# Optimization experiments

Hardware: AMD Instinct MI355X
Metric: run time of the kernel (lower is better)

The kernel has to match this reference:

```python
import jax, jax.numpy as jnp
import numpy as np

NUM_HEADS = 8
SIZES = [(80, 80), (40, 40), (20, 20), (10, 10), (5, 5)]


def _ln(x, g, b):
    m = x.mean(-1, keepdims=True)
    var = ((x - m) ** 2).mean(-1, keepdims=True)
    return (x - m) / jnp.sqrt(var + 1e-5) * g + b


def setup_inputs() -> dict:
    key = jax.random.key(0)
    ks = jax.random.split(key, 24)
    bs, c, S = 2, 256, 1024  # v_dim = embed_dim = c
    d = {}
    for i, (h, w) in enumerate(SIZES):
        d[f"q{i}"] = jax.random.normal(ks[i], (bs, c, h, w), jnp.float32)
    d["cache"] = jax.random.normal(ks[5], (bs, S, c), jnp.float32)
    d["mask"] = jax.random.randint(ks[6], (bs, S), 0, 2).astype(jnp.int32)
    d["ln_v_g"] = jnp.ones((c,), jnp.float32)
    d["ln_v_b"] = jnp.zeros((c,), jnp.float32)
    d["ln_c_g"] = jnp.ones((c,), jnp.float32)
    d["ln_c_b"] = jnp.zeros((c,), jnp.float32)
    sd = c ** -0.5
    d["Wv"] = jax.random.normal(ks[7], (c, c), jnp.float32) * sd
    d["bv"] = jnp.zeros((c,), jnp.float32)
    d["Wc"] = jax.random.normal(ks[8], (c, c), jnp.float32) * sd
    d["bc"] = jnp.zeros((c,), jnp.float32)
    d["Wvc"] = jax.random.normal(ks[9], (c, c), jnp.float32) * sd
    d["bvc"] = jnp.zeros((c,), jnp.float32)
    d["Wo"] = jax.random.normal(ks[10], (c, c), jnp.float32) * sd
    d["bo"] = jnp.zeros((c,), jnp.float32)
    d["Wg1"] = jax.random.normal(ks[11], (c, c // 2), jnp.float32) * sd
    d["bg1"] = jnp.zeros((c // 2,), jnp.float32)
    d["Wg2"] = jax.random.normal(ks[12], (c // 2, c), jnp.float32) * 0.01
    d["bg2"] = jnp.zeros((c,), jnp.float32)
    return d


def _forward(q0, q1, q2, q3, q4, cache, mask, ln_v_g, ln_v_b, ln_c_g, ln_c_b,
             Wv, bv, Wc, bc, Wvc, bvc, Wo, bo, Wg1, bg1, Wg2, bg2):
    feats = [q0, q1, q2, q3, q4]
    bs = q0.shape[0]
    sizes = [(f.shape[2], f.shape[3]) for f in feats]
    # permute_and_flatten: (bs, c, h, w) -> (bs, h*w, c), concat over levels
    v = jnp.concatenate(
        [f.reshape(bs, f.shape[1], -1).transpose(0, 2, 1) for f in feats], axis=1)
    T = v.shape[1]
    E = Wv.shape[1]
    hd = E // NUM_HEADS
    scale = hd ** -0.5

    vn = _ln(v, ln_v_g, ln_v_b)
    cn = _ln(cache, ln_c_g, ln_c_b)

    q = ((vn @ Wv + bv) * scale).reshape(bs, T, NUM_HEADS, hd).transpose(0, 2, 1, 3)
    k = (cn @ Wc + bc).reshape(bs, -1, NUM_HEADS, hd).transpose(0, 2, 1, 3)
    val = (cn @ Wvc + bvc).reshape(bs, -1, NUM_HEADS, hd).transpose(0, 2, 1, 3)

    attn = jnp.einsum('bhtd,bhsd->bhts', q, k)
    attn = jnp.clip(attn, -50000.0, 50000.0)
    mf = mask.astype(attn.dtype)  # (bs, S); zeros -> -9e15, ones kept as +1.0 (faithful)
    attn = attn + jnp.where(mf == 0, jnp.asarray(-9e15, attn.dtype), mf)[:, None, None, :]
    p = jax.nn.softmax(attn, axis=-1)  # dropout inactive in eval mode

    o = jnp.einsum('bhts,bhsd->bhtd', p, val).transpose(0, 2, 1, 3).reshape(bs, T, E)
    delta = o @ Wo + bo

    gate = jnp.tanh(jax.nn.relu(v @ Wg1 + bg1) @ Wg2 + bg2)
    new_v = (v + gate * delta).transpose(0, 2, 1)  # (bs, c, T)

    outs = []
    start = 0
    for h, w in sizes:
        outs.append(new_v[:, :, start:start + h * w].reshape(bs, -1, h, w))
        start += h * w
    return tuple(outs)


def reference(q0, q1, q2, q3, q4, cache, mask, ln_v_g, ln_v_b, ln_c_g, ln_c_b,
              Wv, bv, Wc, bc, Wvc, bvc, Wo, bo, Wg1, bg1, Wg2, bg2):
    return _forward(q0, q1, q2, q3, q4, cache, mask, ln_v_g, ln_v_b, ln_c_g, ln_c_b,
                    Wv, bv, Wc, bc, Wvc, bvc, Wo, bo, Wg1, bg1, Wg2, bg2)
```

## Files before the change

### kernel.cpp

```cpp
#include <hip/hip_runtime.h>
#include <hip/hip_bf16.h>
#include <math.h>


typedef __attribute__((ext_vector_type(8))) short short8;
typedef __attribute__((ext_vector_type(4))) float f32x4;
typedef __hip_bfloat16 bf16;

#define T_TOK 8525
#define S_TOK 1024
#define CDIM  256
#define NHEAD 8
#define BSZ   2

static __device__ __forceinline__ f32x4 mfma16(short8 a, short8 b, f32x4 c) {
  return __builtin_amdgcn_mfma_f32_16x16x32_bf16(a, b, c, 0, 0, 0);
}

static __device__ __forceinline__ float fexp2(float x) {
#if __has_builtin(__builtin_amdgcn_exp2f)
  return __builtin_amdgcn_exp2f(x);
#else
  return exp2f(x);
#endif
}

static __device__ __forceinline__ unsigned int pack_bf16(float a, float b) {
#if __has_builtin(__builtin_amdgcn_perm)
  return __builtin_amdgcn_perm(__float_as_uint(b), __float_as_uint(a), 0x07060302u);
#else
  return (__float_as_uint(a) >> 16) | (__float_as_uint(b) & 0xFFFF0000u);
#endif
}

__global__ __launch_bounds__(256) void prep_misc(
    const float* __restrict__ Wv, const float* __restrict__ Wc,
    const float* __restrict__ Wvc, const float* __restrict__ Wo,
    const float* __restrict__ Wg1, const float* __restrict__ Wg2,
    const float* __restrict__ bc, const float* __restrict__ bvc,
    const float* __restrict__ cache, const float* __restrict__ ln_c_g,
    const float* __restrict__ ln_c_b,
    bf16* __restrict__ WvT, bf16* __restrict__ WcvcT, bf16* __restrict__ WoT,
    bf16* __restrict__ Wg1T, bf16* __restrict__ Wg2T, float* __restrict__ biasCV,
    bf16* __restrict__ cnb) {
  const int bid = blockIdx.x, tid = threadIdx.x;
  if (bid == 80) {
    biasCV[tid] = bc[tid];
    biasCV[tid + 256] = bvc[tid];
    return;
  }
  if (bid > 80) {
    int lane = tid & 63;
    int row = (bid - 81) * 4 + (tid >> 6);
    const float* x = cache + (size_t)row * CDIM;
    float v0 = x[lane], v1 = x[lane + 64], v2 = x[lane + 128], v3 = x[lane + 192];
    float s = v0 + v1 + v2 + v3;
    float s2 = v0 * v0 + v1 * v1 + v2 * v2 + v3 * v3;
#pragma unroll
    for (int off = 1; off < 64; off <<= 1) {
      s += __shfl_xor(s, off);
      s2 += __shfl_xor(s2, off);
    }
    float mean = s * (1.f / 256.f);
    float var = s2 * (1.f / 256.f) - mean * mean;
    float rstd = rsqrtf(var + 1e-5f);
    bf16* y = cnb + (size_t)row * CDIM;
    y[lane] = __float2bfloat16((v0 - mean) * rstd * ln_c_g[lane] + ln_c_b[lane]);
    y[lane + 64] = __float2bfloat16((v1 - mean) * rstd * ln_c_g[lane + 64] + ln_c_b[lane + 64]);
    y[lane + 128] = __float2bfloat16((v2 - mean) * rstd * ln_c_g[lane + 128] + ln_c_b[lane + 128]);
    y[lane + 192] = __float2bfloat16((v3 - mean) * rstd * ln_c_g[lane + 192] + ln_c_b[lane + 192]);
    return;
  }
  const float* W; bf16* WT; int K, N, local;
  if (bid < 16)      { W = Wv;  WT = WvT;           K = 256; N = 256; local = bid; }
  else if (bid < 32) { W = Wc;  WT = WcvcT;         K = 256; N = 256; local = bid - 16; }
  else if (bid < 48) { W = Wvc; WT = WcvcT + 65536; K = 256; N = 256; local = bid - 32; }
  else if (bid < 64) { W = Wo;  WT = WoT;           K = 256; N = 256; local = bid - 48; }
  else if (bid < 72) { W = Wg1; WT = Wg1T;          K = 256; N = 128; local = bid - 64; }
  else               { W = Wg2; WT = Wg2T;          K = 128; N = 256; local = bid - 72; }
  const int ktiles = K >> 6;
  const int K0 = (local % ktiles) * 64, N0 = (local / ktiles) * 64;
  __shared__ float tl[64][65];
  const int kk = tid >> 4, n4 = (tid & 15) * 4;
#pragma unroll
  for (int i = 0; i < 4; ++i) {
    int k = kk + 16 * i;
    float4 w4 = *(const float4*)&W[(size_t)(K0 + k) * N + N0 + n4];
    tl[n4 + 0][k] = w4.x; tl[n4 + 1][k] = w4.y;
    tl[n4 + 2][k] = w4.z; tl[n4 + 3][k] = w4.w;
  }
  __syncthreads();
  const int nn = tid >> 4, k4 = (tid & 15) * 4;
#pragma unroll
  for (int i = 0; i < 4; ++i) {
    int n = nn + 16 * i;
    bf16 o[4] __attribute__((aligned(8)));
#pragma unroll
    for (int j = 0; j < 4; ++j) o[j] = __float2bfloat16(tl[n][k4 + j]);
    *(uint2*)&WT[(size_t)(N0 + n) * K + K0 + k4] = *(uint2*)o;
  }
}

__global__ __launch_bounds__(256) void build_v_ln(
    const float* __restrict__ q0, const float* __restrict__ q1,
    const float* __restrict__ q2, const float* __restrict__ q3,
    const float* __restrict__ q4, const float* __restrict__ g,
    const float* __restrict__ beta, float* __restrict__ vT,
    bf16* __restrict__ vb, bf16* __restrict__ vnb) {
  constexpr int HW[5] = {6400, 1600, 400, 100, 25};
  constexpr int TST[5] = {0, 6400, 8000, 8400, 8500};
  constexpr int T16[5] = {0, 400, 500, 525, 532};
  __shared__ float tile[16][260];
  const int tid = threadIdx.x;
  const int tileid = blockIdx.x, b = blockIdx.y;
  int lvl = 0;
#pragma unroll
  for (int i = 1; i < 5; ++i) if (tileid >= T16[i]) lvl = i;
  const int p0 = (tileid - T16[lvl]) * 16;
  const int hw = HW[lvl];
  const float* src = ((lvl == 0) ? q0 : (lvl == 1) ? q1 : (lvl == 2) ? q2
                      : (lvl == 3) ? q3 : q4) + (size_t)b * CDIM * hw;
  const int pl = tid & 15, cb = tid >> 4;
  const int pg = p0 + pl;
#pragma unroll
  for (int i = 0; i < 16; ++i) {
    int c = cb + 16 * i;
    tile[pl][c] = (pg < hw) ? src[(size_t)c * hw + pg] : 0.f;
  }
  __syncthreads();
  if (pg < hw) {
    int tglob = TST[lvl] + pg;
#pragma unroll
    for (int i = 0; i < 16; ++i) {
      int c = cb + 16 * i;
      vT[((size_t)b * CDIM + c) * T_TOK + tglob] = tile[pl][c];
    }
  }
  const int lane = tid & 63, w = tid >> 6;
#pragma unroll
  for (int rr = 0; rr < 4; ++rr) {
    int row = w * 4 + rr;
    int p = p0 + row;
    if (p >= hw) continue;
    float x0 = tile[row][lane], x1 = tile[row][lane + 64],
          x2 = tile[row][lane + 128], x3 = tile[row][lane + 192];
    float s = x0 + x1 + x2 + x3;
    float s2 = x0 * x0 + x1 * x1 + x2 * x2 + x3 * x3;
#pragma unroll
    for (int off = 1; off < 64; off <<= 1) {
      s += __shfl_xor(s, off);
      s2 += __shfl_xor(s2, off);
    }
    float mean = s * (1.f / 256.f);
    float var = s2 * (1.f / 256.f) - mean * mean;
    float rstd = rsqrtf(var + 1e-5f);
    size_t base = ((size_t)b * T_TOK + TST[lvl] + p) * CDIM;
    float xs[4] = {x0, x1, x2, x3};
#pragma unroll
    for (int j = 0; j < 4; ++j) {
      int c = lane + 64 * j;
      float x = xs[j];
      vb[base + c] = __float2bfloat16(x);
      vnb[base + c] = __float2bfloat16((x - mean) * rstd * g[c] + beta[c]);
    }
  }
}

template <int K, int EPI>
__global__ __launch_bounds__(256) void gemm_nt(
    const bf16* __restrict__ A, const bf16* __restrict__ WT,
    const float* __restrict__ bias, void* __restrict__ out,
    float* __restrict__ auxD, int M) {
  __shared__ __align__(16) bf16 Asl[128][136];
  __shared__ __align__(16) bf16 Bsl[64][136];
  const int tid = threadIdx.x;
  const int wave = tid >> 6, lane = tid & 63, quad = lane >> 4, l15 = lane & 15;
  const int m0 = blockIdx.y * 128;
  const int n0 = blockIdx.x * 64;
  f32x4 acc[2][4];
#pragma unroll
  for (int i = 0; i < 2; ++i)
#pragma unroll
    for (int j = 0; j < 4; ++j) acc[i][j] = (f32x4){0.f, 0.f, 0.f, 0.f};

  for (int k0 = 0; k0 < K; k0 += 128) {
    __syncthreads();
#pragma unroll
    for (int c = 0; c < 8; ++c) {
      int chunk = c * 256 + tid;
      int row = chunk >> 4, col = (chunk & 15) * 8;
      int gr = m0 + row;
      if (gr >= M) gr = M - 1;
      *(uint4*)&Asl[row][col] = *(const uint4*)&A[(size_t)gr * K + k0 + col];
    }
#pragma unroll
    for (int c = 0; c < 4; ++c) {
      int chunk = c * 256 + tid;
      int row = chunk >> 4, col = (chunk & 15) * 8;
      *(uint4*)&Bsl[row][col] = *(const uint4*)&WT[(size_t)(n0 + row) * K + k0 + col];
    }
    __syncthreads();
#pragma unroll
    for (int kk = 0; kk < 128; kk += 32) {
      short8 af0 = *(const short8*)&Asl[wave * 32 + l15][kk + quad * 8];
      short8 af1 = *(const short8*)&Asl[wave * 32 + 16 + l15][kk + quad * 8];
      short8 bf0 = *(const short8*)&Bsl[l15][kk + quad * 8];
      short8 bf1 = *(const short8*)&Bsl[16 + l15][kk + quad * 8];
      short8 bf2 = *(const short8*)&Bsl[32 + l15][kk + quad * 8];
      short8 bf3 = *(const short8*)&Bsl[48 + l15][kk + quad * 8];
      acc[0][0] = mfma16(af0, bf0, acc[0][0]);
      acc[0][1] = mfma16(af0, bf1, acc[0][1]);
      acc[0][2] = mfma16(af0, bf2, acc[0][2]);
      acc[0][3] = mfma16(af0, bf3, acc[0][3]);
      acc[1][0] = mfma16(af1, bf0, acc[1][0]);
      acc[1][1] = mfma16(af1, bf1, acc[1][1]);
      acc[1][2] = mfma16(af1, bf2, acc[1][2]);
      acc[1][3] = mfma16(af1, bf3, acc[1][3]);
    }
  }
  const int ldN = gridDim.x * 64;
#pragma unroll
  for (int ms = 0; ms < 2; ++ms)
#pragma unroll
    for (int nt = 0; nt < 4; ++nt)
#pragma unroll
      for (int r = 0; r < 4; ++r) {
        int m = m0 + wave * 32 + ms * 16 + quad * 4 + r;
        if (m >= M) continue;
        int n = n0 + nt * 16 + l15;
        float x = acc[ms][nt][r] + bias[n];
        if (EPI == 0) {
          ((bf16*)out)[(size_t)m * ldN + n] = __float2bfloat16(x * 0.25504765517f);
        } else if (EPI == 4) {
          ((bf16*)out)[(size_t)m * ldN + n] = __float2bfloat16(fmaxf(x, 0.f));
        } else {
          if (n < 256) {
            ((bf16*)out)[(size_t)m * 256 + n] = __float2bfloat16(x);
          } else {
            int n2 = n - 256;
            int bb = m >> 10, s = m & 1023;
            int hh = n2 >> 5, d = n2 & 31;
            ((bf16*)auxD)[(((size_t)(bb * NHEAD + hh) * 32 + d) << 10) + s] =
                __float2bfloat16(x);
          }
        }
      }
}

__global__ __launch_bounds__(512) void attn_kernel(
    const bf16* __restrict__ qb, const bf16* __restrict__ kb,
    const bf16* __restrict__ valTb, const int* __restrict__ mask,
    bf16* __restrict__ ob) {
  __shared__ __align__(16) bf16 Ksl[2][4096];
  __shared__ __align__(16) bf16 Vsl[2][4096];
  __shared__ __align__(16) float biasl[2][128];
  const int tid = threadIdx.x;
  const int wv = tid >> 6, lane = tid & 63, quad = lane >> 4, l15 = lane & 15;
  const int b = blockIdx.y >> 3, h = blockIdx.y & 7;
  const int t0w = blockIdx.x * 128 + wv * 16;
  int t_load = t0w + l15;
  if (t_load >= T_TOK) t_load = T_TOK - 1;
  short8 qf = *(const short8*)&qb[((size_t)b * T_TOK + t_load) * CDIM + h * 32 + quad * 8];
  f32x4 o0 = (f32x4){0.f, 0.f, 0.f, 0.f};
  f32x4 o1 = (f32x4){0.f, 0.f, 0.f, 0.f};
  f32x4 o2 = (f32x4){0.f, 0.f, 0.f, 0.f};
  const short8 ones = (short8){0x3F80, 0x3F80, 0x3F80, 0x3F80,
                               0x3F80, 0x3F80, 0x3F80, 0x3F80};
  const size_t kbase = ((size_t)b * S_TOK) * CDIM + h * 32;
  const size_t vbase = (size_t)(b * NHEAD + h) << 15;
  const int ks = tid >> 2, kd16 = tid & 3;
  const int kdst = (ks >> 4) * 512 + (ks & 15) * 32 + kd16 * 8;
  const int vd = tid >> 4, vs8 = (tid & 15) * 8;
  const int P0tab[4] = {0, 16, 4, 20};
  const int p1 = (vs8 >> 5) * 32 + P0tab[(vs8 >> 3) & 3];
  const int p2 = p1 + 8;
  const int vx = vd & 7;
  const int vo1 = vd * 128 + (((p1 >> 3) ^ vx) << 3) + (p1 & 7);
  const int vo2 = vd * 128 + (((p2 >> 3) ^ vx) << 3) + (p2 & 7);
  const int rx = l15 & 7;

  uint4 kreg = *(const uint4*)&kb[kbase + (size_t)ks * CDIM + kd16 * 8];
  uint4 vreg = *(const uint4*)&valTb[vbase + ((size_t)vd << 10) + vs8];
  float breg = 0.f;
  if (tid < 128) breg = mask[b * S_TOK + tid] ? -12.984255368f : -1e18f;
  *(uint4*)&Ksl[0][kdst] = kreg;
  {
    uint2 lo; lo.x = vreg.x; lo.y = vreg.y;
    uint2 hi; hi.x = vreg.z; hi.y = vreg.w;
    *(uint2*)&Vsl[0][vo1] = lo;
    *(uint2*)&Vsl[0][vo2] = hi;
  }
  if (tid < 128) biasl[0][tid] = breg;
  __syncthreads();

  for (int sbi = 0; sbi < 8; ++sbi) {
    const int cur = sbi & 1;
    if (sbi < 7) {
      int sb = (sbi + 1) * 128;
      kreg = *(const uint4*)&kb[kbase + (size_t)(sb + ks) * CDIM + kd16 * 8];
      vreg = *(const uint4*)&valTb[vbase + ((size_t)vd << 10) + sb + vs8];
      if (tid < 128) breg = mask[b * S_TOK + sb + tid] ? -12.984255368f : -1e18f;
    }
#pragma unroll
    for (int ss = 0; ss < 128; ss += 32) {
      short8 kf0 = *(const short8*)&Ksl[cur][(ss >> 4) * 512 + l15 * 32 + quad * 8];
      short8 kf1 = *(const short8*)&Ksl[cur][(ss >> 4) * 512 + 512 + l15 * 32 + quad * 8];
      f32x4 bias0 = *(const f32x4*)&biasl[cur][ss + quad * 4];
      f32x4 bias1 = *(const f32x4*)&biasl[cur][ss + 16 + quad * 4];
      f32x4 s0 = mfma16(kf0, qf, bias0);
      f32x4 s1 = mfma16(kf1, qf, bias1);
      float pa = fexp2(s0[0]), pb = fexp2(s0[1]);
      float pc = fexp2(s0[2]), pd = fexp2(s0[3]);
      float pe = fexp2(s1[0]), pf_ = fexp2(s1[1]);
      float pg = fexp2(s1[2]), ph = fexp2(s1[3]);
      uint4 pu;
      pu.x = pack_bf16(pa, pb);
      pu.y = pack_bf16(pc, pd);
      pu.z = pack_bf16(pe, pf_);
      pu.w = pack_bf16(pg, ph);
      short8 pfr = *(short8*)&pu;
      int vc = (ss >> 3) + quad;
      short8 vf0 = *(const short8*)&Vsl[cur][l15 * 128 + ((vc ^ rx) << 3)];
      short8 vf1 = *(const short8*)&Vsl[cur][(16 + l15) * 128 + ((vc ^ rx) << 3)];
      o2 = mfma16(pfr, ones, o2);
      o0 = mfma16(pfr, vf0, o0);
      o1 = mfma16(pfr, vf1, o1);
    }
    if (sbi < 7) {
      const int nxt = cur ^ 1;
      *(uint4*)&Ksl[nxt][kdst] = kreg;
      uint2 lo; lo.x = vreg.x; lo.y = vreg.y;
      uint2 hi; hi.x = vreg.z; hi.y = vreg.w;
      *(uint2*)&Vsl[nxt][vo1] = lo;
      *(uint2*)&Vsl[nxt][vo2] = hi;
      if (tid < 128) biasl[nxt][tid] = breg;
    }
    __syncthreads();
  }
#pragma unroll
  for (int r = 0; r < 4; ++r) {
    int t = t0w + quad * 4 + r;
    if (t < T_TOK) {
      float rli = 1.0f / o2[r];
      size_t basep = ((size_t)b * T_TOK + t) * CDIM + h * 32;
      ob[basep + l15] = __float2bfloat16(o0[r] * rli);
      ob[basep + 16 + l15] = __float2bfloat16(o1[r] * rli);
    }
  }
}

__global__ __launch_bounds__(256) void gemm_out(
    const bf16* __restrict__ obuf, const bf16* __restrict__ WoT,
    const float* __restrict__ bo, const bf16* __restrict__ ghb,
    const bf16* __restrict__ Wg2T, const float* __restrict__ bg2,
    const float* __restrict__ vT, float* __restrict__ out, int M) {
  constexpr int HW[5] = {6400, 1600, 400, 100, 25};
  constexpr int TST[5] = {0, 6400, 8000, 8400, 8500};
  constexpr size_t OUTOFF[5] = {0, 3276800, 4096000, 4300800, 4352000};
  __shared__ __align__(16) char smem[52224];
  bf16 (*Asl)[136] = (bf16(*)[136])smem;
  bf16 (*Bsl)[136] = (bf16(*)[136])(smem + 34816);
  float (*tile)[132] = (float(*)[132])smem;
  const int tid = threadIdx.x;
  const int wave = tid >> 6, lane = tid & 63, quad = lane >> 4, l15 = lane & 15;
  const int m0 = blockIdx.y * 128, n0 = blockIdx.x * 64;
  f32x4 aD[2][4], aG[2][4];
#pragma unroll
  for (int i = 0; i < 2; ++i)
#pragma unroll
    for (int j = 0; j < 4; ++j) {
      aD[i][j] = (f32x4){0.f, 0.f, 0.f, 0.f};
      aG[i][j] = (f32x4){0.f, 0.f, 0.f, 0.f};
    }
  for (int k0 = 0; k0 < 256; k0 += 128) {
    __syncthreads();
#pragma unroll
    for (int c = 0; c < 8; ++c) {
      int chunk = c * 256 + tid;
      int row = chunk >> 4, col = (chunk & 15) * 8;
      int gr = m0 + row;
      if (gr >= M) gr = M - 1;
      *(uint4*)&Asl[row][col] = *(const uint4*)&obuf[(size_t)gr * 256 + k0 + col];
    }
#pragma unroll
    for (int c = 0; c < 4; ++c) {
      int chunk = c * 256 + tid;
      int row = chunk >> 4, col = (chunk & 15) * 8;
      *(uint4*)&Bsl[row][col] = *(const uint4*)&WoT[(size_t)(n0 + row) * 256 + k0 + col];
    }
    __syncthreads();
#pragma unroll
    for (int kk = 0; kk < 128; kk += 32) {
      short8 af0 = *(const short8*)&Asl[wave * 32 + l15][kk + quad * 8];
      short8 af1 = *(const short8*)&Asl[wave * 32 + 16 + l15][kk + quad * 8];
#pragma unroll
      for (int j = 0; j < 4; ++j) {
        short8 bfj = *(const short8*)&Bsl[j * 16 + l15][kk + quad * 8];
        aD[0][j] = mfma16(af0, bfj, aD[0][j]);
        aD[1][j] = mfma16(af1, bfj, aD[1][j]);
      }
    }
  }
  __syncthreads();
#pragma unroll
  for (int c = 0; c < 8; ++c) {
    int chunk = c * 256 + tid;
    int row = chunk >> 4, col = (chunk & 15) * 8;
    int gr = m0 + row;
    if (gr >= M) gr = M - 1;
    *(uint4*)&Asl[row][col] = *(const uint4*)&ghb[(size_t)gr * 128 + col];
  }
#pragma unroll
  for (int c = 0; c < 4; ++c) {
    int chunk = c * 256 + tid;
    int row = chunk >> 4, col = (chunk & 15) * 8;
    *(uint4*)&Bsl[row][col] = *(const uint4*)&Wg2T[(size_t)(n0 + row) * 128 + col];
  }
  __syncthreads();
#pragma unroll
  for (int kk = 0; kk < 128; kk += 32) {
    short8 af0 = *(const short8*)&Asl[wave * 32 + l15][kk + quad * 8];
    short8 af1 = *(const short8*)&Asl[wave * 32 + 16 + l15][kk + quad * 8];
#pragma unroll
    for (int j = 0; j < 4; ++j) {
      short8 bfj = *(const short8*)&Bsl[j * 16 + l15][kk + quad * 8];
      aG[0][j] = mfma16(af0, bfj, aG[0][j]);
      aG[1][j] = mfma16(af1, bfj, aG[1][j]);
    }
  }
  __syncthreads();
#pragma unroll
  for (int ms = 0; ms < 2; ++ms)
#pragma unroll
    for (int nt = 0; nt < 4; ++nt) {
      int n = n0 + nt * 16 + l15;
      float bod = bo[n], bgd = bg2[n];
      float4 res;
      float tmp[4];
#pragma unroll
      for (int r = 0; r < 4; ++r) {
        float xd = aD[ms][nt][r] + bod;
        float xg = aG[ms][nt][r] + bgd;
        float xc = fminf(fmaxf(xg, -15.f), 15.f);
        float e = __expf(2.f * xc);
        float gt = (e - 1.f) / (e + 1.f);
        tmp[r] = gt * xd;
      }
      res.x = tmp[0]; res.y = tmp[1]; res.z = tmp[2]; res.w = tmp[3];
      *(float4*)&tile[nt * 16 + l15][wave * 32 + ms * 16 + quad * 4] = res;
    }
  __syncthreads();
  const int tl = tid & 127, c2 = tid >> 7;
  const int t = m0 + tl;
  const bool valid = t < M;
  int bb = (t >= T_TOK) ? 1 : 0;
  int tt = t - bb * T_TOK;
  if (tt >= T_TOK) tt = T_TOK - 1;
  int lvl = 0;
#pragma unroll
  for (int i = 1; i < 5; ++i) if (tt >= TST[i]) lvl = i;
  const int p = tt - TST[lvl], hw = HW[lvl];
  float* dst = out + OUTOFF[lvl] + ((size_t)bb * CDIM + n0) * hw + p;
  const float* vsrc = vT + ((size_t)bb * CDIM + n0) * T_TOK + tt;
#pragma unroll
  for (int c0 = 0; c0 < 32; ++c0) {
    int c = c0 * 2 + c2;
    if (valid) dst[(size_t)c * hw] = vsrc[(size_t)c * T_TOK] + tile[c][tl];
  }
}

extern "C" void kernel_launch(void* const* d_in, const int* in_sizes, int n_in,
                              void* d_out, int out_size, void* d_ws, size_t ws_size,
                              hipStream_t stream) {
  const float* q0 = (const float*)d_in[0];
  const float* q1 = (const float*)d_in[1];
  const float* q2 = (const float*)d_in[2];
  const float* q3 = (const float*)d_in[3];
  const float* q4 = (const float*)d_in[4];
  const float* cache = (const float*)d_in[5];
  const int* mask = (const int*)d_in[6];
  const float* ln_v_g = (const float*)d_in[7];
  const float* ln_v_b = (const float*)d_in[8];
  const float* ln_c_g = (const float*)d_in[9];
  const float* ln_c_b = (const float*)d_in[10];
  const float* Wv = (const float*)d_in[11];
  const float* bv = (const float*)d_in[12];
  const float* Wc = (const float*)d_in[13];
  const float* bc = (const float*)d_in[14];
  const float* Wvc = (const float*)d_in[15];
  const float* bvc = (const float*)d_in[16];
  const float* Wo = (const float*)d_in[17];
  const float* bo = (const float*)d_in[18];
  const float* Wg1 = (const float*)d_in[19];
  const float* bg1 = (const float*)d_in[20];
  const float* Wg2 = (const float*)d_in[21];
  const float* bg2 = (const float*)d_in[22];
  float* out = (float*)d_out;

  const int R = BSZ * T_TOK;
  const size_t RC = (size_t)R * CDIM;
  const size_t SC = (size_t)BSZ * S_TOK * CDIM;

  char* p = (char*)d_ws;
  float* vT = (float*)p;           p += RC * 4;
  bf16* vb = (bf16*)p;             p += RC * 2;
  bf16* vnb = (bf16*)p;            p += RC * 2;
  bf16* qb = (bf16*)p;             p += RC * 2;
  bf16* ob = (bf16*)p;             p += RC * 2;
  bf16* ghb = (bf16*)p;            p += (size_t)R * 128 * 2;
  bf16* cnb = (bf16*)p;            p += SC * 2;
  bf16* kb = (bf16*)p;             p += SC * 2;
  bf16* valTb = (bf16*)p;          p += SC * 2;
  bf16* WvT = (bf16*)p;            p += 65536 * 2;
  bf16* WcvcT = (bf16*)p;          p += 131072 * 2;
  bf16* WoT = (bf16*)p;            p += 65536 * 2;
  bf16* Wg1T = (bf16*)p;           p += 32768 * 2;
  bf16* Wg2T = (bf16*)p;           p += 32768 * 2;
  float* biasCV = (float*)p;       p += 512 * 4;

  prep_misc<<<dim3(593), dim3(256), 0, stream>>>(
      Wv, Wc, Wvc, Wo, Wg1, Wg2, bc, bvc, cache, ln_c_g, ln_c_b,
      WvT, WcvcT, WoT, Wg1T, Wg2T, biasCV, cnb);
  build_v_ln<<<dim3(534, BSZ), dim3(256), 0, stream>>>(
      q0, q1, q2, q3, q4, ln_v_g, ln_v_b, vT, vb, vnb);
  gemm_nt<256, 0><<<dim3(4, 134), dim3(256), 0, stream>>>(
      vnb, WvT, bv, qb, nullptr, R);
  gemm_nt<256, 6><<<dim3(8, 16), dim3(256), 0, stream>>>(
      cnb, WcvcT, biasCV, kb, (float*)valTb, BSZ * S_TOK);
  gemm_nt<256, 4><<<dim3(2, 134), dim3(256), 0, stream>>>(
      vb, Wg1T, bg1, ghb, nullptr, R);
  attn_kernel<<<dim3(67, BSZ * NHEAD), dim3(512), 0, stream>>>(
      qb, kb, valTb, mask, ob);
  gemm_out<<<dim3(4, 134), dim3(256), 0, stream>>>(
      ob, WoT, bo, ghb, Wg2T, bg2, vT, out, R);
}
```

Baseline: 216.7 us.

## Merge prep kernels, fuse Q and gate GEMMs, double query tiles per attention wave

Merges the weight-transpose/cache-LN kernel and the v-build/LN kernel into one launch. Merges the Q projection and the first gate GEMM into a single GEMM launch over a concatenated weight, choosing the A operand per column block. Restructures attention so each wave handles 32 query rows with 256-thread blocks, reusing each K/V fragment for two query groups. Together these cut launch count and shared-memory reloads of K/V, at the cost of higher register pressure in attention.

```diff
diff --git a/kernel.cpp b/kernel.cpp
--- a/kernel.cpp
+++ b/kernel.cpp
@@ -33,23 +33,32 @@
 #endif
 }
 
-__global__ __launch_bounds__(256) void prep_misc(
+__global__ __launch_bounds__(256) void stage1(
+    const float* __restrict__ q0, const float* __restrict__ q1,
+    const float* __restrict__ q2, const float* __restrict__ q3,
+    const float* __restrict__ q4,
     const float* __restrict__ Wv, const float* __restrict__ Wc,
     const float* __restrict__ Wvc, const float* __restrict__ Wo,
     const float* __restrict__ Wg1, const float* __restrict__ Wg2,
+    const float* __restrict__ bv, const float* __restrict__ bg1,
     const float* __restrict__ bc, const float* __restrict__ bvc,
     const float* __restrict__ cache, const float* __restrict__ ln_c_g,
-    const float* __restrict__ ln_c_b,
-    bf16* __restrict__ WvT, bf16* __restrict__ WcvcT, bf16* __restrict__ WoT,
-    bf16* __restrict__ Wg1T, bf16* __restrict__ Wg2T, float* __restrict__ biasCV,
-    bf16* __restrict__ cnb) {
+    const float* __restrict__ ln_c_b, const float* __restrict__ ln_v_g,
+    const float* __restrict__ ln_v_b,
+    bf16* __restrict__ WqgT, bf16* __restrict__ WcvcT, bf16* __restrict__ WoT,
+    bf16* __restrict__ Wg2T, float* __restrict__ biasCV,
+    float* __restrict__ biasQG, bf16* __restrict__ cnb,
+    float* __restrict__ vT, bf16* __restrict__ vb, bf16* __restrict__ vnb) {
+  __shared__ float sm[4160];
   const int bid = blockIdx.x, tid = threadIdx.x;
   if (bid == 80) {
     biasCV[tid] = bc[tid];
     biasCV[tid + 256] = bvc[tid];
+    biasQG[tid] = bv[tid];
+    if (tid < 128) biasQG[256 + tid] = bg1[tid];
     return;
   }
-  if (bid > 80) {
+  if (bid > 80 && bid < 593) {
     int lane = tid & 63;
     int row = (bid - 81) * 4 + (tid >> 6);
     const float* x = cache + (size_t)row * CDIM;
@@ -71,48 +80,43 @@
     y[lane + 192] = __float2bfloat16((v3 - mean) * rstd * ln_c_g[lane + 192] + ln_c_b[lane + 192]);
     return;
   }
-  const float* W; bf16* WT; int K, N, local;
-  if (bid < 16)      { W = Wv;  WT = WvT;           K = 256; N = 256; local = bid; }
-  else if (bid < 32) { W = Wc;  WT = WcvcT;         K = 256; N = 256; local = bid - 16; }
-  else if (bid < 48) { W = Wvc; WT = WcvcT + 65536; K = 256; N = 256; local = bid - 32; }
-  else if (bid < 64) { W = Wo;  WT = WoT;           K = 256; N = 256; local = bid - 48; }
-  else if (bid < 72) { W = Wg1; WT = Wg1T;          K = 256; N = 128; local = bid - 64; }
-  else               { W = Wg2; WT = Wg2T;          K = 128; N = 256; local = bid - 72; }
-  const int ktiles = K >> 6;
-  const int K0 = (local % ktiles) * 64, N0 = (local / ktiles) * 64;
-  __shared__ float tl[64][65];
-  const int kk = tid >> 4, n4 = (tid & 15) * 4;
-#pragma unroll
-  for (int i = 0; i < 4; ++i) {
-    int k = kk + 16 * i;
-    float4 w4 = *(const float4*)&W[(size_t)(K0 + k) * N + N0 + n4];
-    tl[n4 + 0][k] = w4.x; tl[n4 + 1][k] = w4.y;
-    tl[n4 + 2][k] = w4.z; tl[n4 + 3][k] = w4.w;
-  }
-  __syncthreads();
-  const int nn = tid >> 4, k4 = (tid & 15) * 4;
-#pragma unroll
-  for (int i = 0; i < 4; ++i) {
-    int n = nn + 16 * i;
-    bf16 o[4] __attribute__((aligned(8)));
-#pragma unroll
-    for (int j = 0; j < 4; ++j) o[j] = __float2bfloat16(tl[n][k4 + j]);
-    *(uint2*)&WT[(size_t)(N0 + n) * K + K0 + k4] = *(uint2*)o;
-  }
-}
-
-__global__ __launch_bounds__(256) void build_v_ln(
-    const float* __restrict__ q0, const float* __restrict__ q1,
-    const float* __restrict__ q2, const float* __restrict__ q3,
-    const float* __restrict__ q4, const float* __restrict__ g,
-    const float* __restrict__ beta, float* __restrict__ vT,
-    bf16* __restrict__ vb, bf16* __restrict__ vnb) {
+  if (bid < 80) {
+    float (*tl)[65] = (float(*)[65])sm;
+    const float* W; bf16* WT; int K, N, local;
+    if (bid < 16)      { W = Wv;  WT = WqgT;           K = 256; N = 256; local = bid; }
+    else if (bid < 32) { W = Wc;  WT = WcvcT;          K = 256; N = 256; local = bid - 16; }
+    else if (bid < 48) { W = Wvc; WT = WcvcT + 65536;  K = 256; N = 256; local = bid - 32; }
+    else if (bid < 64) { W = Wo;  WT = WoT;            K = 256; N = 256; local = bid - 48; }
+    else if (bid < 72) { W = Wg1; WT = WqgT + 65536;   K = 256; N = 128; local = bid - 64; }
+    else               { W = Wg2; WT = Wg2T;           K = 128; N = 256; local = bid - 72; }
+    const int ktiles = K >> 6;
+    const int K0 = (local % ktiles) * 64, N0 = (local / ktiles) * 64;
+    const int kk = tid >> 4, n4 = (tid & 15) * 4;
+#pragma unroll
+    for (int i = 0; i < 4; ++i) {
+      int k = kk + 16 * i;
+      float4 w4 = *(const float4*)&W[(size_t)(K0 + k) * N + N0 + n4];
+      tl[n4 + 0][k] = w4.x; tl[n4 + 1][k] = w4.y;
+      tl[n4 + 2][k] = w4.z; tl[n4 + 3][k] = w4.w;
+    }
+    __syncthreads();
+    const int nn = tid >> 4, k4 = (tid & 15) * 4;
+#pragma unroll
+    for (int i = 0; i < 4; ++i) {
+      int n = nn + 16 * i;
+      bf16 o[4] __attribute__((aligned(8)));
+#pragma unroll
+      for (int j = 0; j < 4; ++j) o[j] = __float2bfloat16(tl[n][k4 + j]);
+      *(uint2*)&WT[(size_t)(N0 + n) * K + K0 + k4] = *(uint2*)o;
+    }
+    return;
+  }
   constexpr int HW[5] = {6400, 1600, 400, 100, 25};
   constexpr int TST[5] = {0, 6400, 8000, 8400, 8500};
   constexpr int T16[5] = {0, 400, 500, 525, 532};
-  __shared__ float tile[16][260];
-  const int tid = threadIdx.x;
-  const int tileid = blockIdx.x, b = blockIdx.y;
+  float (*tile)[260] = (float(*)[260])sm;
+  const int bb = bid - 593;
+  const int tileid = bb % 534, b = bb / 534;
   int lvl = 0;
 #pragma unroll
   for (int i = 1; i < 5; ++i) if (tileid >= T16[i]) lvl = i;
@@ -161,29 +165,29 @@
       int c = lane + 64 * j;
       float x = xs[j];
       vb[base + c] = __float2bfloat16(x);
-      vnb[base + c] = __float2bfloat16((x - mean) * rstd * g[c] + beta[c]);
-    }
-  }
-}
-
-template <int K, int EPI>
-__global__ __launch_bounds__(256) void gemm_nt(
-    const bf16* __restrict__ A, const bf16* __restrict__ WT,
-    const float* __restrict__ bias, void* __restrict__ out,
-    float* __restrict__ auxD, int M) {
+      vnb[base + c] = __float2bfloat16((x - mean) * rstd * ln_v_g[c] + ln_v_b[c]);
+    }
+  }
+}
+
+__global__ __launch_bounds__(256) void gemm_qg(
+    const bf16* __restrict__ vnb, const bf16* __restrict__ vb,
+    const bf16* __restrict__ WqgT, const float* __restrict__ biasQG,
+    bf16* __restrict__ qb, bf16* __restrict__ ghb, int M) {
   __shared__ __align__(16) bf16 Asl[128][136];
   __shared__ __align__(16) bf16 Bsl[64][136];
   const int tid = threadIdx.x;
   const int wave = tid >> 6, lane = tid & 63, quad = lane >> 4, l15 = lane & 15;
   const int m0 = blockIdx.y * 128;
   const int n0 = blockIdx.x * 64;
+  const bf16* A = (n0 < 256) ? vnb : vb;
   f32x4 acc[2][4];
 #pragma unroll
   for (int i = 0; i < 2; ++i)
 #pragma unroll
     for (int j = 0; j < 4; ++j) acc[i][j] = (f32x4){0.f, 0.f, 0.f, 0.f};
 
-  for (int k0 = 0; k0 < K; k0 += 128) {
+  for (int k0 = 0; k0 < 256; k0 += 128) {
     __syncthreads();
 #pragma unroll
     for (int c = 0; c < 8; ++c) {
@@ -191,13 +195,13 @@
       int row = chunk >> 4, col = (chunk & 15) * 8;
       int gr = m0 + row;
       if (gr >= M) gr = M - 1;
-      *(uint4*)&Asl[row][col] = *(const uint4*)&A[(size_t)gr * K + k0 + col];
+      *(uint4*)&Asl[row][col] = *(const uint4*)&A[(size_t)gr * 256 + k0 + col];
     }
 #pragma unroll
     for (int c = 0; c < 4; ++c) {
       int chunk = c * 256 + tid;
       int row = chunk >> 4, col = (chunk & 15) * 8;
-      *(uint4*)&Bsl[row][col] = *(const uint4*)&WT[(size_t)(n0 + row) * K + k0 + col];
+      *(uint4*)&Bsl[row][col] = *(const uint4*)&WqgT[(size_t)(n0 + row) * 256 + k0 + col];
     }
     __syncthreads();
 #pragma unroll
@@ -218,7 +222,6 @@
       acc[1][3] = mfma16(af1, bf3, acc[1][3]);
     }
   }
-  const int ldN = gridDim.x * 64;
 #pragma unroll
   for (int ms = 0; ms < 2; ++ms)
 #pragma unroll
@@ -228,26 +231,85 @@
         int m = m0 + wave * 32 + ms * 16 + quad * 4 + r;
         if (m >= M) continue;
         int n = n0 + nt * 16 + l15;
-        float x = acc[ms][nt][r] + bias[n];
-        if (EPI == 0) {
-          ((bf16*)out)[(size_t)m * ldN + n] = __float2bfloat16(x * 0.25504765517f);
-        } else if (EPI == 4) {
-          ((bf16*)out)[(size_t)m * ldN + n] = __float2bfloat16(fmaxf(x, 0.f));
+        float x = acc[ms][nt][r] + biasQG[n];
+        if (n < 256) {
+          qb[(size_t)m * 256 + n] = __float2bfloat16(x * 0.25504765517f);
         } else {
-          if (n < 256) {
-            ((bf16*)out)[(size_t)m * 256 + n] = __float2bfloat16(x);
-          } else {
-            int n2 = n - 256;
-            int bb = m >> 10, s = m & 1023;
-            int hh = n2 >> 5, d = n2 & 31;
-            ((bf16*)auxD)[(((size_t)(bb * NHEAD + hh) * 32 + d) << 10) + s] =
-                __float2bfloat16(x);
-          }
+          ghb[(size_t)m * 128 + (n - 256)] = __float2bfloat16(fmaxf(x, 0.f));
         }
       }
 }
 
-__global__ __launch_bounds__(512) void attn_kernel(
+__global__ __launch_bounds__(256) void gemm_kval(
+    const bf16* __restrict__ cnb, const bf16* __restrict__ WcvcT,
+    const float* __restrict__ biasCV, bf16* __restrict__ kb,
+    bf16* __restrict__ valTb, int M) {
+  __shared__ __align__(16) bf16 Asl[128][136];
+  __shared__ __align__(16) bf16 Bsl[64][136];
+  const int tid = threadIdx.x;
+  const int wave = tid >> 6, lane = tid & 63, quad = lane >> 4, l15 = lane & 15;
+  const int m0 = blockIdx.y * 128;
+  const int n0 = blockIdx.x * 64;
+  f32x4 acc[2][4];
+#pragma unroll
+  for (int i = 0; i < 2; ++i)
+#pragma unroll
+    for (int j = 0; j < 4; ++j) acc[i][j] = (f32x4){0.f, 0.f, 0.f, 0.f};
+
+  for (int k0 = 0; k0 < 256; k0 += 128) {
+    __syncthreads();
+#pragma unroll
+    for (int c = 0; c < 8; ++c) {
+      int chunk = c * 256 + tid;
+      int row = chunk >> 4, col = (chunk & 15) * 8;
+      *(uint4*)&Asl[row][col] = *(const uint4*)&cnb[(size_t)(m0 + row) * 256 + k0 + col];
+    }
+#pragma unroll
+    for (int c = 0; c < 4; ++c) {
+      int chunk = c * 256 + tid;
+      int row = chunk >> 4, col = (chunk & 15) * 8;
+      *(uint4*)&Bsl[row][col] = *(const uint4*)&WcvcT[(size_t)(n0 + row) * 256 + k0 + col];
+    }
+    __syncthreads();
+#pragma unroll
+    for (int kk = 0; kk < 128; kk += 32) {
+      short8 af0 = *(const short8*)&Asl[wave * 32 + l15][kk + quad * 8];
+      short8 af1 = *(const short8*)&Asl[wave * 32 + 16 + l15][kk + quad * 8];
+      short8 bf0 = *(const short8*)&Bsl[l15][kk + quad * 8];
+      short8 bf1 = *(const short8*)&Bsl[16 + l15][kk + quad * 8];
+      short8 bf2 = *(const short8*)&Bsl[32 + l15][kk + quad * 8];
+      short8 bf3 = *(const short8*)&Bsl[48 + l15][kk + quad * 8];
+      acc[0][0] = mfma16(af0, bf0, acc[0][0]);
+      acc[0][1] = mfma16(af0, bf1, acc[0][1]);
+      acc[0][2] = mfma16(af0, bf2, acc[0][2]);
+      acc[0][3] = mfma16(af0, bf3, acc[0][3]);
+      acc[1][0] = mfma16(af1, bf0, acc[1][0]);
+      acc[1][1] = mfma16(af1, bf1, acc[1][1]);
+      acc[1][2] = mfma16(af1, bf2, acc[1][2]);
+      acc[1][3] = mfma16(af1, bf3, acc[1][3]);
+    }
+  }
+#pragma unroll
+  for (int ms = 0; ms < 2; ++ms)
+#pragma unroll
+    for (int nt = 0; nt < 4; ++nt)
+#pragma unroll
+      for (int r = 0; r < 4; ++r) {
+        int m = m0 + wave * 32 + ms * 16 + quad * 4 + r;
+        int n = n0 + nt * 16 + l15;
+        float x = acc[ms][nt][r] + biasCV[n];
+        if (n < 256) {
+          kb[(size_t)m * 256 + n] = __float2bfloat16(x);
+        } else {
+          int n2 = n - 256;
+          int bb = m >> 10, s = m & 1023;
+          int hh = n2 >> 5, d = n2 & 31;
+          valTb[(((size_t)(bb * NHEAD + hh) * 32 + d) << 10) + s] = __float2bfloat16(x);
+        }
+      }
+}
+
+__global__ __launch_bounds__(256) void attn_kernel(
     const bf16* __restrict__ qb, const bf16* __restrict__ kb,
     const bf16* __restrict__ valTb, const int* __restrict__ mask,
     bf16* __restrict__ ob) {
@@ -257,38 +319,51 @@
   const int tid = threadIdx.x;
   const int wv = tid >> 6, lane = tid & 63, quad = lane >> 4, l15 = lane & 15;
   const int b = blockIdx.y >> 3, h = blockIdx.y & 7;
-  const int t0w = blockIdx.x * 128 + wv * 16;
-  int t_load = t0w + l15;
-  if (t_load >= T_TOK) t_load = T_TOK - 1;
-  short8 qf = *(const short8*)&qb[((size_t)b * T_TOK + t_load) * CDIM + h * 32 + quad * 8];
-  f32x4 o0 = (f32x4){0.f, 0.f, 0.f, 0.f};
-  f32x4 o1 = (f32x4){0.f, 0.f, 0.f, 0.f};
-  f32x4 o2 = (f32x4){0.f, 0.f, 0.f, 0.f};
+  const int t0w = blockIdx.x * 128 + wv * 32;
+  int tA = t0w + l15;       if (tA >= T_TOK) tA = T_TOK - 1;
+  int tB = t0w + 16 + l15;  if (tB >= T_TOK) tB = T_TOK - 1;
+  short8 qf0 = *(const short8*)&qb[((size_t)b * T_TOK + tA) * CDIM + h * 32 + quad * 8];
+  short8 qf1 = *(const short8*)&qb[((size_t)b * T_TOK + tB) * CDIM + h * 32 + quad * 8];
+  f32x4 o0a = {0.f, 0.f, 0.f, 0.f}, o1a = {0.f, 0.f, 0.f, 0.f}, o2a = {0.f, 0.f, 0.f, 0.f};
+  f32x4 o0b = {0.f, 0.f, 0.f, 0.f}, o1b = {0.f, 0.f, 0.f, 0.f}, o2b = {0.f, 0.f, 0.f, 0.f};
   const short8 ones = (short8){0x3F80, 0x3F80, 0x3F80, 0x3F80,
                                0x3F80, 0x3F80, 0x3F80, 0x3F80};
   const size_t kbase = ((size_t)b * S_TOK) * CDIM + h * 32;
   const size_t vbase = (size_t)(b * NHEAD + h) << 15;
-  const int ks = tid >> 2, kd16 = tid & 3;
-  const int kdst = (ks >> 4) * 512 + (ks & 15) * 32 + kd16 * 8;
-  const int vd = tid >> 4, vs8 = (tid & 15) * 8;
   const int P0tab[4] = {0, 16, 4, 20};
-  const int p1 = (vs8 >> 5) * 32 + P0tab[(vs8 >> 3) & 3];
-  const int p2 = p1 + 8;
-  const int vx = vd & 7;
-  const int vo1 = vd * 128 + (((p1 >> 3) ^ vx) << 3) + (p1 & 7);
-  const int vo2 = vd * 128 + (((p2 >> 3) ^ vx) << 3) + (p2 & 7);
+  int kdst[2], vo1[2], vo2[2];
+  size_t kofs[2], vofs[2];
+#pragma unroll
+  for (int c = 0; c < 2; ++c) {
+    int chunk = c * 256 + tid;
+    int ks = chunk >> 2, kd16 = chunk & 3;
+    kdst[c] = (ks >> 4) * 512 + (ks & 15) * 32 + kd16 * 8;
+    kofs[c] = (size_t)ks * CDIM + kd16 * 8;
+    int vd = chunk >> 4, vs8 = (chunk & 15) * 8;
+    int p1 = (vs8 >> 5) * 32 + P0tab[(vs8 >> 3) & 3];
+    int p2 = p1 + 8;
+    int vx = vd & 7;
+    vo1[c] = vd * 128 + (((p1 >> 3) ^ vx) << 3) + (p1 & 7);
+    vo2[c] = vd * 128 + (((p2 >> 3) ^ vx) << 3) + (p2 & 7);
+    vofs[c] = ((size_t)vd << 10) + vs8;
+  }
   const int rx = l15 & 7;
 
-  uint4 kreg = *(const uint4*)&kb[kbase + (size_t)ks * CDIM + kd16 * 8];
-  uint4 vreg = *(const uint4*)&valTb[vbase + ((size_t)vd << 10) + vs8];
+  uint4 kreg[2], vreg[2];
   float breg = 0.f;
+#pragma unroll
+  for (int c = 0; c < 2; ++c) {
+    kreg[c] = *(const uint4*)&kb[kbase + kofs[c]];
+    vreg[c] = *(const uint4*)&valTb[vbase + vofs[c]];
+  }
   if (tid < 128) breg = mask[b * S_TOK + tid] ? -12.984255368f : -1e18f;
-  *(uint4*)&Ksl[0][kdst] = kreg;
-  {
-    uint2 lo; lo.x = vreg.x; lo.y = vreg.y;
-    uint2 hi; hi.x = vreg.z; hi.y = vreg.w;
-    *(uint2*)&Vsl[0][vo1] = lo;
-    *(uint2*)&Vsl[0][vo2] = hi;
+#pragma unroll
+  for (int c = 0; c < 2; ++c) {
+    *(uint4*)&Ksl[0][kdst[c]] = kreg[c];
+    uint2 lo; lo.x = vreg[c].x; lo.y = vreg[c].y;
+    uint2 hi; hi.x = vreg[c].z; hi.y = vreg[c].w;
+    *(uint2*)&Vsl[0][vo1[c]] = lo;
+    *(uint2*)&Vsl[0][vo2[c]] = hi;
   }
   if (tid < 128) biasl[0][tid] = breg;
   __syncthreads();
@@ -297,8 +372,11 @@
     const int cur = sbi & 1;
     if (sbi < 7) {
       int sb = (sbi + 1) * 128;
-      kreg = *(const uint4*)&kb[kbase + (size_t)(sb + ks) * CDIM + kd16 * 8];
-      vreg = *(const uint4*)&valTb[vbase + ((size_t)vd << 10) + sb + vs8];
+#pragma unroll
+      for (int c = 0; c < 2; ++c) {
+        kreg[c] = *(const uint4*)&kb[kbase + (size_t)sb * CDIM + kofs[c]];
+        vreg[c] = *(const uint4*)&valTb[vbase + sb + vofs[c]];
+      }
       if (tid < 128) breg = mask[b * S_TOK + sb + tid] ? -12.984255368f : -1e18f;
     }
 #pragma unroll
@@ -307,44 +385,68 @@
       short8 kf1 = *(const short8*)&Ksl[cur][(ss >> 4) * 512 + 512 + l15 * 32 + quad * 8];
       f32x4 bias0 = *(const f32x4*)&biasl[cur][ss + quad * 4];
       f32x4 bias1 = *(const f32x4*)&biasl[cur][ss + 16 + quad * 4];
-      f32x4 s0 = mfma16(kf0, qf, bias0);
-      f32x4 s1 = mfma16(kf1, qf, bias1);
-      float pa = fexp2(s0[0]), pb = fexp2(s0[1]);
-      float pc = fexp2(s0[2]), pd = fexp2(s0[3]);
-      float pe = fexp2(s1[0]), pf_ = fexp2(s1[1]);
-      float pg = fexp2(s1[2]), ph = fexp2(s1[3]);
-      uint4 pu;
-      pu.x = pack_bf16(pa, pb);
-      pu.y = pack_bf16(pc, pd);
-      pu.z = pack_bf16(pe, pf_);
-      pu.w = pack_bf16(pg, ph);
-      short8 pfr = *(short8*)&pu;
       int vc = (ss >> 3) + quad;
       short8 vf0 = *(const short8*)&Vsl[cur][l15 * 128 + ((vc ^ rx) << 3)];
       short8 vf1 = *(const short8*)&Vsl[cur][(16 + l15) * 128 + ((vc ^ rx) << 3)];
-      o2 = mfma16(pfr, ones, o2);
-      o0 = mfma16(pfr, vf0, o0);
-      o1 = mfma16(pfr, vf1, o1);
+      {
+        f32x4 s0 = mfma16(kf0, qf0, bias0);
+        f32x4 s1 = mfma16(kf1, qf0, bias1);
+        float pa = fexp2(s0[0]), pb = fexp2(s0[1]);
+        float pc = fexp2(s0[2]), pd = fexp2(s0[3]);
+        float pe = fexp2(s1[0]), pf_ = fexp2(s1[1]);
+        float pg = fexp2(s1[2]), ph = fexp2(s1[3]);
+        uint4 pu;
+        pu.x = pack_bf16(pa, pb); pu.y = pack_bf16(pc, pd);
+        pu.z = pack_bf16(pe, pf_); pu.w = pack_bf16(pg, ph);
+        short8 pfr = *(short8*)&pu;
+        o2a = mfma16(pfr, ones, o2a);
+        o0a = mfma16(pfr, vf0, o0a);
+        o1a = mfma16(pfr, vf1, o1a);
+      }
+      {
+        f32x4 s0 = mfma16(kf0, qf1, bias0);
+        f32x4 s1 = mfma16(kf1, qf1, bias1);
+        float pa = fexp2(s0[0]), pb = fexp2(s0[1]);
+        float pc = fexp2(s0[2]), pd = fexp2(s0[3]);
+        float pe = fexp2(s1[0]), pf_ = fexp2(s1[1]);
+        float pg = fexp2(s1[2]), ph = fexp2(s1[3]);
+        uint4 pu;
+        pu.x = pack_bf16(pa, pb); pu.y = pack_bf16(pc, pd);
+        pu.z = pack_bf16(pe, pf_); pu.w = pack_bf16(pg, ph);
+        short8 pfr = *(short8*)&pu;
+        o2b = mfma16(pfr, ones, o2b);
+        o0b = mfma16(pfr, vf0, o0b);
+        o1b = mfma16(pfr, vf1, o1b);
+      }
     }
     if (sbi < 7) {
       const int nxt = cur ^ 1;
-      *(uint4*)&Ksl[nxt][kdst] = kreg;
-      uint2 lo; lo.x = vreg.x; lo.y = vreg.y;
-      uint2 hi; hi.x = vreg.z; hi.y = vreg.w;
-      *(uint2*)&Vsl[nxt][vo1] = lo;
-      *(uint2*)&Vsl[nxt][vo2] = hi;
+#pragma unroll
+      for (int c = 0; c < 2; ++c) {
+        *(uint4*)&Ksl[nxt][kdst[c]] = kreg[c];
+        uint2 lo; lo.x = vreg[c].x; lo.y = vreg[c].y;
+        uint2 hi; hi.x = vreg[c].z; hi.y = vreg[c].w;
+        *(uint2*)&Vsl[nxt][vo1[c]] = lo;
+        *(uint2*)&Vsl[nxt][vo2[c]] = hi;
+      }
       if (tid < 128) biasl[nxt][tid] = breg;
     }
     __syncthreads();
   }
 #pragma unroll
-  for (int r = 0; r < 4; ++r) {
-    int t = t0w + quad * 4 + r;
-    if (t < T_TOK) {
-      float rli = 1.0f / o2[r];
-      size_t basep = ((size_t)b * T_TOK + t) * CDIM + h * 32;
-      ob[basep + l15] = __float2bfloat16(o0[r] * rli);
-      ob[basep + 16 + l15] = __float2bfloat16(o1[r] * rli);
+  for (int g = 0; g < 2; ++g) {
+    f32x4 o0 = g ? o0b : o0a;
+    f32x4 o1 = g ? o1b : o1a;
+    f32x4 o2 = g ? o2b : o2a;
+#pragma unroll
+    for (int r = 0; r < 4; ++r) {
+      int t = t0w + g * 16 + quad * 4 + r;
+      if (t < T_TOK) {
+        float rli = 1.0f / o2[r];
+        size_t basep = ((size_t)b * T_TOK + t) * CDIM + h * 32;
+        ob[basep + l15] = __float2bfloat16(o0[r] * rli);
+        ob[basep + 16 + l15] = __float2bfloat16(o1[r] * rli);
+      }
     }
   }
 }
@@ -511,25 +613,22 @@
   bf16* cnb = (bf16*)p;            p += SC * 2;
   bf16* kb = (bf16*)p;             p += SC * 2;
   bf16* valTb = (bf16*)p;          p += SC * 2;
-  bf16* WvT = (bf16*)p;            p += 65536 * 2;
+  bf16* WqgT = (bf16*)p;           p += 98304 * 2;
   bf16* WcvcT = (bf16*)p;          p += 131072 * 2;
   bf16* WoT = (bf16*)p;            p += 65536 * 2;
-  bf16* Wg1T = (bf16*)p;           p += 32768 * 2;
   bf16* Wg2T = (bf16*)p;           p += 32768 * 2;
   float* biasCV = (float*)p;       p += 512 * 4;
-
-  prep_misc<<<dim3(593), dim3(256), 0, stream>>>(
-      Wv, Wc, Wvc, Wo, Wg1, Wg2, bc, bvc, cache, ln_c_g, ln_c_b,
-      WvT, WcvcT, WoT, Wg1T, Wg2T, biasCV, cnb);
-  build_v_ln<<<dim3(534, BSZ), dim3(256), 0, stream>>>(
-      q0, q1, q2, q3, q4, ln_v_g, ln_v_b, vT, vb, vnb);
-  gemm_nt<256, 0><<<dim3(4, 134), dim3(256), 0, stream>>>(
-      vnb, WvT, bv, qb, nullptr, R);
-  gemm_nt<256, 6><<<dim3(8, 16), dim3(256), 0, stream>>>(
-      cnb, WcvcT, biasCV, kb, (float*)valTb, BSZ * S_TOK);
-  gemm_nt<256, 4><<<dim3(2, 134), dim3(256), 0, stream>>>(
-      vb, Wg1T, bg1, ghb, nullptr, R);
-  attn_kernel<<<dim3(67, BSZ * NHEAD), dim3(512), 0, stream>>>(
+  float* biasQG = (float*)p;       p += 384 * 4;
+
+  stage1<<<dim3(1661), dim3(256), 0, stream>>>(
+      q0, q1, q2, q3, q4, Wv, Wc, Wvc, Wo, Wg1, Wg2, bv, bg1, bc, bvc,
+      cache, ln_c_g, ln_c_b, ln_v_g, ln_v_b,
+      WqgT, WcvcT, WoT, Wg2T, biasCV, biasQG, cnb, vT, vb, vnb);
+  gemm_qg<<<dim3(6, 134), dim3(256), 0, stream>>>(
+      vnb, vb, WqgT, biasQG, qb, ghb, R);
+  gemm_kval<<<dim3(8, 16), dim3(256), 0, stream>>>(
+      cnb, WcvcT, biasCV, kb, valTb, BSZ * S_TOK);
+  attn_kernel<<<dim3(67, BSZ * NHEAD), dim3(256), 0, stream>>>(
       qb, kb, valTb, mask, ob);
   gemm_out<<<dim3(4, 134), dim3(256), 0, stream>>>(
       ob, WoT, bo, ghb, Wg2T, bg2, vT, out, R);
```

Result: faster. 210.7 us (-2.8%).
